# Kernel optimization log

Hardware: AMD Instinct MI355X
Metric: run time of the kernel (lower is better)

Reference implementation:

```python
import math
import jax, jax.numpy as jnp
import numpy as np

L, NH, DF = 4, 4, 32  # num_layers, num_heads, head_dim (H=128)
EPS = 1e-5


def ln(x, g, b):
    m = x.mean(-1, keepdims=True)
    v = ((x - m) ** 2).mean(-1, keepdims=True)
    return (x - m) * jax.lax.rsqrt(v + EPS) * g + b


def mha(x, w_in, b_in, w_out, b_out):
    # torch nn.MultiheadAttention self-attention, batch_first, no mask
    B, S, H = x.shape
    q, k, v = jnp.split(x @ w_in + b_in, 3, axis=-1)
    q = q.reshape(B, S, NH, DF)
    k = k.reshape(B, S, NH, DF)
    v = v.reshape(B, S, NH, DF)
    s = jnp.einsum('bqhd,bkhd->bhqk', q, k) / math.sqrt(DF)
    a = jax.nn.softmax(s, axis=-1)
    o = jnp.einsum('bhqk,bkhd->bqhd', a, v).reshape(B, S, H)
    return o @ w_out + b_out


def _forward(X_k, time_embed, step_embed, W_tr, b_tr, W_in, b_in, g_in, be_in,
             W_e, b_e, aw, ab, ow, ob, tng, tnb, f1w, f1b, f2w, f2b, fng, fnb,
             Wq, Wk, Wv, Wo, bo, Wem, bem, Wea, bea, e1w, e1b, e2w, e2b,
             gng, gnb, eng, enb, W_out, b_out, k_index, edge_index):
    B, N, T1, Cin = X_k.shape
    H = W_in.shape[1]
    # --- precompute_graph: self-loops + structural edge features ---
    loop = jnp.arange(N, dtype=edge_index.dtype)
    ei = jnp.concatenate([edge_index, jnp.stack([loop, loop])], axis=1)
    dst, src = ei[0], ei[1]
    E = ei.shape[1]
    deg = jnp.zeros((N,), jnp.float32).at[dst].add(1.0)
    deg_max = jnp.maximum(deg.max(), 1.0)
    edge_w = 1.0 / jnp.maximum(deg[dst], 1.0)
    feat = jnp.stack([edge_w, deg[src] / deg_max, deg[dst] / deg_max], axis=1)  # [E,3]
    # --- input embedding ---
    t_emb = time_embed  # [T1, te] (lookup of arange(T1) = whole table)
    X = jnp.concatenate(
        [X_k, jnp.broadcast_to(t_emb[None, None], (B, N, T1, t_emb.shape[-1]))], axis=-1)
    h = ln(X @ W_in + b_in, g_in, be_in)
    h = h + step_embed[k_index][:, None, None, :]
    e = feat @ W_e + b_e                       # [E, de]
    t_re = t_emb @ W_tr + b_tr                 # [T1, H]
    BT = B * T1
    for l in range(L):
        # temporal attention over T1
        h_flat = h.reshape(B * N, T1, H)
        attn_out = mha(h_flat, aw[l], ab[l], ow[l], ob[l])
        h = ln(h + attn_out.reshape(B, N, T1, H), tng[l], tnb[l])
        ffn = jax.nn.gelu(h @ f1w[l] + f1b[l], approximate=False) @ f2w[l] + f2b[l]
        h = ln(h + ffn, fng[l], fnb[l])
        h = h + t_re[None, None]
        # DiGress GT sparse graph block over N
        h_BT = h.transpose(0, 2, 1, 3).reshape(BT, N, H)
        Q = (h_BT @ Wq[l]).reshape(BT, N, NH, DF)
        K = (h_BT @ Wk[l]).reshape(BT, N, NH, DF)
        V = (h_BT @ Wv[l]).reshape(BT, N, NH, DF)
        scores = (Q[:, dst] * K[:, src]).sum(-1) / math.sqrt(DF)  # [BT,E,NH]
        scores = scores * (e @ Wem[l] + bem[l] + 1.0) + (e @ Wea[l] + bea[l])
        s_max = jax.lax.stop_gradient(scores.max(axis=1, keepdims=True))
        exp_s = jnp.exp(scores - s_max)
        denom = jnp.zeros((BT, N, NH), exp_s.dtype).at[:, dst, :].add(exp_s)
        attn = exp_s / (denom[:, dst, :] + 1e-9)
        agg = (attn[..., None] * V[:, src]).reshape(BT, E, H)
        out = jnp.zeros((BT, N, H), h.dtype).at[:, dst, :].add(agg)
        h_BT = h_BT + out @ Wo[l] + bo[l]
        h_mean = jax.lax.stop_gradient(h_BT).mean(0)               # [N,H]
        e_in = jnp.concatenate([h_mean[dst], h_mean[src], e], axis=-1)
        e_mlp = jax.nn.gelu(e_in @ e1w[l] + e1b[l], approximate=False) @ e2w[l] + e2b[l]
        e = ln(e + e_mlp, eng[l], enb[l])
        h = ln(h_BT.reshape(B, T1, N, H).transpose(0, 2, 1, 3), gng[l], gnb[l])
    return jax.nn.softmax(h @ W_out + b_out, axis=-1)


def setup_inputs() -> dict:
    key = jax.random.key(0)
    B, N, T1 = 2, 2000, 12
    sd, cc, te, H, de, nh = 4, 2, 16, 128, 16, 4
    Cin = (1 + cc) * sd  # 12
    E0, max_steps = 32000, 1024
    ks = iter(jax.random.split(key, 60))
    def rn(*shape, s=0.05):
        return jax.random.normal(next(ks), shape, jnp.float32) * s
    z = lambda *s: jnp.zeros(s, jnp.float32)
    o = lambda *s: jnp.ones(s, jnp.float32)
    return dict(
        X_k=jax.random.normal(next(ks), (B, N, T1, Cin), jnp.float32),
        time_embed=rn(T1, te), step_embed=rn(max_steps, H),
        W_tr=rn(te, H), b_tr=z(H),
        W_in=rn(Cin + te, H), b_in=z(H), g_in=o(H), be_in=z(H),
        W_e=rn(3, de), b_e=z(de),
        aw=rn(L, H, 3 * H), ab=z(L, 3 * H), ow=rn(L, H, H), ob=z(L, H),
        tng=o(L, H), tnb=z(L, H),
        f1w=rn(L, H, 2 * H), f1b=z(L, 2 * H), f2w=rn(L, 2 * H, H), f2b=z(L, H),
        fng=o(L, H), fnb=z(L, H),
        Wq=rn(L, H, H), Wk=rn(L, H, H), Wv=rn(L, H, H),
        Wo=rn(L, H, H), bo=z(L, H),
        Wem=rn(L, de, nh), bem=z(L, nh), Wea=rn(L, de, nh), bea=z(L, nh),
        e1w=rn(L, 2 * H + de, 4 * de), e1b=z(L, 4 * de),
        e2w=rn(L, 4 * de, de), e2b=z(L, de),
        gng=o(L, H), gnb=z(L, H), eng=o(L, de), enb=z(L, de),
        W_out=rn(H, sd), b_out=z(sd),
        k_index=jax.random.randint(next(ks), (B,), 0, max_steps),
        edge_index=jax.random.randint(next(ks), (2, E0), 0, N),
    )


def reference(X_k, time_embed, step_embed, W_tr, b_tr, W_in, b_in, g_in, be_in,
              W_e, b_e, aw, ab, ow, ob, tng, tnb, f1w, f1b, f2w, f2b, fng, fnb,
              Wq, Wk, Wv, Wo, bo, Wem, bem, Wea, bea, e1w, e1b, e2w, e2b,
              gng, gnb, eng, enb, W_out, b_out, k_index, edge_index):
    return _forward(X_k, time_embed, step_embed, W_tr, b_tr, W_in, b_in, g_in, be_in,
                    W_e, b_e, aw, ab, ow, ob, tng, tnb, f1w, f1b, f2w, f2b, fng, fnb,
                    Wq, Wk, Wv, Wo, bo, Wem, bem, Wea, bea, e1w, e1b, e2w, e2b,
                    gng, gnb, eng, enb, W_out, b_out, k_index, edge_index)
```

## Files before the change

### kernel.cpp

```cpp
#include <hip/hip_runtime.h>
#include <math.h>

#define NN 2000
#define T1C 12
#define BBC 2
#define HHC 128
#define NHD 4
#define DFD 32
#define LLC 4
#define DEC 16
#define TEC 16
#define CINC 12
#define E0C 32000
#define EEC 34000
#define BTC 24
#define MROWS 48000
#define EPSLN 1e-5f
#define SCALEQK 0.17677669529663687f

typedef __attribute__((ext_vector_type(8))) short short8;
typedef __attribute__((ext_vector_type(4))) float f32x4;


__device__ __forceinline__ unsigned short f2b(float f)
{
    unsigned u = __float_as_uint(f);
    return (unsigned short)((u + 0x7FFF + ((u >> 16) & 1)) >> 16);
}

__device__ __forceinline__ float b2f(unsigned short h)
{
    return __uint_as_float(((unsigned)h) << 16);
}


__global__ __launch_bounds__(256) void convwp_k(const float* __restrict__ W, unsigned short* __restrict__ Bp,
                                                int LN_, int K, int N, int noff, int Ntot)
{
    int idx = blockIdx.x * blockDim.x + threadIdx.x;
    int total = LN_ * K * N;
    if (idx >= total) return;
    int l = idx / (K * N);
    int r = idx - l * (K * N);
    int k = r / N;
    int n = r - k * N + noff;
    size_t off = (size_t)l * K * Ntot +
                 ((size_t)((n >> 4) * (K >> 5) + (k >> 5)) << 9) +
                 (((k >> 3) & 3) << 7) + ((n & 15) << 3) + (k & 7);
    Bp[off] = f2b(W[idx]);
}

__global__ __launch_bounds__(256) void convw12_k(const float* __restrict__ e1w, unsigned short* __restrict__ W12P)
{
    int idx = blockIdx.x * blockDim.x + threadIdx.x;
    if (idx >= LLC * 128 * 128) return;
    int l = idx >> 14;
    int r = idx & 16383;
    int c = r >> 7, k = r & 127;
    int sk = (c < 64) ? k : k + 128;
    int sc = c & 63;
    W12P[idx] = f2b(e1w[((size_t)l * 272 + sk) * 64 + sc]);
}

__global__ __launch_bounds__(256) void convwoT_k(const float* __restrict__ Wo, unsigned short* __restrict__ WoT)
{
    int idx = blockIdx.x * blockDim.x + threadIdx.x;
    if (idx >= LLC * 128 * 128) return;
    int l = idx >> 14;
    int r = idx & 16383;
    int c = r >> 7, k = r & 127;
    WoT[idx] = f2b(Wo[((size_t)l * 128 + k) * 128 + c]);
}


template<int K, int EPI, int OUTM>
__global__ __launch_bounds__(256) void gemm2_k(
    const unsigned short* __restrict__ A, const unsigned short* __restrict__ Bp,
    const float* __restrict__ bias, float* __restrict__ C, unsigned short* __restrict__ Cb,
    const float* __restrict__ res, const float* __restrict__ gam, const float* __restrict__ bet,
    const float* __restrict__ trep,
    int M, int Ntot)
{
    __shared__ unsigned short A_s[128 * 16 * 8];
    __shared__ float red2[2][128][2];

    int tid = threadIdx.x;
    int w = tid >> 6, lane = tid & 63;
    int wr = w & 1, wc = w >> 1;
    int quad = lane >> 4, lr = lane & 15;

    const unsigned short* abase = A + (size_t)blockIdx.x * 128 * K;
    int ntg0 = blockIdx.y * 8 + wc * 4;

    f32x4 acc[4][4];
#pragma unroll
    for (int mt = 0; mt < 4; mt++)
#pragma unroll
        for (int nt = 0; nt < 4; nt++) acc[mt][nt] = (f32x4){0.f, 0.f, 0.f, 0.f};

#pragma unroll
    for (int kb = 0; kb < K; kb += 128) {
        if (kb) __syncthreads();
#pragma unroll
        for (int j = 0; j < 8; j++) {
            int s = j * 256 + tid;
            int row = s >> 4, ks = s & 15;
            int ko = ks ^ (row & 15);
            uint4 d = *(const uint4*)(abase + (size_t)row * K + kb + ko * 8);
            *(uint4*)(A_s + s * 8) = d;
        }
        __syncthreads();
#pragma unroll
        for (int k0 = 0; k0 < 128; k0 += 32) {
            short8 af[4], bf[4];
#pragma unroll
            for (int mt = 0; mt < 4; mt++) {
                int row_l = wr * 64 + mt * 16 + lr;
                int koct = (k0 >> 3) + quad;
                int slot = row_l * 16 + (koct ^ lr);
                af[mt] = *(const short8*)(A_s + slot * 8);
            }
#pragma unroll
            for (int nt = 0; nt < 4; nt++) {
                size_t off = ((size_t)(ntg0 + nt) * (K >> 5) + ((kb + k0) >> 5)) * 512 + lane * 8;
                bf[nt] = *(const short8*)(Bp + off);
            }
#pragma unroll
            for (int mt = 0; mt < 4; mt++)
#pragma unroll
                for (int nt = 0; nt < 4; nt++)
                    acc[mt][nt] = __builtin_amdgcn_mfma_f32_16x16x32_bf16(af[mt], bf[nt], acc[mt][nt], 0, 0, 0);
        }
    }

    int rbase = blockIdx.x * 128 + wr * 64;
    int cbase = blockIdx.y * 128 + wc * 64;

    if constexpr (EPI != 3 && EPI != 4 && EPI != 5) {
#pragma unroll
        for (int mt = 0; mt < 4; mt++) {
#pragma unroll
            for (int nt = 0; nt < 4; nt++) {
                int colg = cbase + nt * 16 + lr;
                float bv = bias ? bias[colg] : 0.f;
#pragma unroll
                for (int i = 0; i < 4; i++) {
                    int row = rbase + mt * 16 + quad * 4 + i;
                    float x = acc[mt][nt][i] + bv;
                    if constexpr (EPI == 1) x = 0.5f * x * (1.f + erff(x * 0.70710678118654752f));
                    if constexpr (EPI == 2) x = res[(size_t)row * Ntot + colg] + x;
                    if constexpr (OUTM & 1) C[(size_t)row * Ntot + colg] = x;
                    if constexpr (OUTM & 4)
                        Cb[(size_t)blockIdx.y * M * 128 + (size_t)row * 128 + (wc * 64 + nt * 16 + lr)] = f2b(x);
                    else if constexpr (OUTM & 2)
                        Cb[(size_t)row * Ntot + colg] = f2b(x);
                }
            }
        }
    } else {
        float s[4][4], s2l[4][4];
#pragma unroll
        for (int mt = 0; mt < 4; mt++)
#pragma unroll
            for (int i = 0; i < 4; i++) { s[mt][i] = 0.f; s2l[mt][i] = 0.f; }
#pragma unroll
        for (int mt = 0; mt < 4; mt++) {
#pragma unroll
            for (int nt = 0; nt < 4; nt++) {
                int colg = cbase + nt * 16 + lr;
                float bv = bias[colg];
#pragma unroll
                for (int i = 0; i < 4; i++) {
                    int row = rbase + mt * 16 + quad * 4 + i;
                    float x = acc[mt][nt][i] + bv + res[(size_t)row * 128 + colg];
                    acc[mt][nt][i] = x;
                    s[mt][i] += x;
                    s2l[mt][i] += x * x;
                }
            }
        }
#pragma unroll
        for (int m = 1; m < 16; m <<= 1) {
#pragma unroll
            for (int mt = 0; mt < 4; mt++)
#pragma unroll
                for (int i = 0; i < 4; i++) {
                    s[mt][i]  += __shfl_xor(s[mt][i], m, 64);
                    s2l[mt][i] += __shfl_xor(s2l[mt][i], m, 64);
                }
        }
        if (lr == 0) {
#pragma unroll
            for (int mt = 0; mt < 4; mt++)
#pragma unroll
                for (int i = 0; i < 4; i++) {
                    int rl = wr * 64 + mt * 16 + quad * 4 + i;
                    red2[wc][rl][0] = s[mt][i];
                    red2[wc][rl][1] = s2l[mt][i];
                }
        }
        __syncthreads();
#pragma unroll
        for (int mt = 0; mt < 4; mt++) {
#pragma unroll
            for (int i = 0; i < 4; i++) {
                int rl = wr * 64 + mt * 16 + quad * 4 + i;
                float st  = red2[0][rl][0] + red2[1][rl][0];
                float s2t = red2[0][rl][1] + red2[1][rl][1];
                float mu = st * (1.f / 128.f);
                float rstd = rsqrtf(s2t * (1.f / 128.f) - mu * mu + EPSLN);
                int row = rbase + mt * 16 + quad * 4 + i;
                if constexpr (EPI == 4) {
                    int t = row % T1C;
                    int bn = row / T1C;
                    int b = bn / NN;
                    int n = bn - b * NN;
                    size_t rowp = (size_t)(b * T1C + t) * NN + n;
                    const float* trow = trep + t * HHC;
#pragma unroll
                    for (int nt = 0; nt < 4; nt++) {
                        int colg = cbase + nt * 16 + lr;
                        float y = (acc[mt][nt][i] - mu) * rstd * gam[colg] + bet[colg] + trow[colg];
                        C[rowp * 128 + colg] = y;
                        Cb[rowp * 128 + colg] = f2b(y);
                    }
                } else if constexpr (EPI == 5) {
                    int bt = row / NN, n = row - bt * NN;
                    int b = bt / T1C, t = bt - b * T1C;
                    size_t rowp = ((size_t)(b * NN + n)) * T1C + t;
#pragma unroll
                    for (int nt = 0; nt < 4; nt++) {
                        int colg = cbase + nt * 16 + lr;
                        float y = (acc[mt][nt][i] - mu) * rstd * gam[colg] + bet[colg];
                        C[rowp * 128 + colg] = y;
                        Cb[rowp * 128 + colg] = f2b(y);
                    }
                } else {
#pragma unroll
                    for (int nt = 0; nt < 4; nt++) {
                        int colg = cbase + nt * 16 + lr;
                        float y = (acc[mt][nt][i] - mu) * rstd * gam[colg] + bet[colg];
                        if constexpr (OUTM & 1) C[(size_t)row * 128 + colg] = y;
                        if constexpr (OUTM & 2) Cb[(size_t)row * 128 + colg] = f2b(y);
                    }
                }
            }
        }
    }
}

template<int K, int EPI, int OUTM>
static void run_gemm2(const unsigned short* A, const unsigned short* Bp, const float* bias,
                      float* C, unsigned short* Cb, const float* res, const float* g, const float* be,
                      const float* trep, int M, int Ntot, hipStream_t stream)
{
    dim3 grid(M / 128, Ntot / 128);
    gemm2_k<K, EPI, OUTM><<<grid, 256, 0, stream>>>(A, Bp, bias, C, Cb, res, g, be, trep, M, Ntot);
}


template<int NT>
__global__ __launch_bounds__(256) void gemm_mfma_k(
    const unsigned short* __restrict__ A, const unsigned short* __restrict__ WT,
    float* __restrict__ C, int M, int K)
{
    const int Nc = NT * 32;
    int tid = threadIdx.x;
    int w = tid >> 6, lane = tid & 63;
    int wr = w & 1, wc = w >> 1;
    int r0 = blockIdx.x * 32 + wr * 16;
    int c0 = wc * NT * 16;
    int lr = lane & 15;
    int kq = (lane >> 4) * 8;
    int arow = r0 + lr; if (arow >= M) arow = M - 1;
    const unsigned short* ap = A + (size_t)arow * K + kq;
    const unsigned short* wp = WT + (size_t)(c0 + lr) * K + kq;

    f32x4 acc[NT];
#pragma unroll
    for (int t = 0; t < NT; t++) acc[t] = (f32x4){0.f, 0.f, 0.f, 0.f};

    for (int k0 = 0; k0 < K; k0 += 32) {
        short8 a = *(const short8*)(ap + k0);
#pragma unroll
        for (int t = 0; t < NT; t++) {
            short8 b = *(const short8*)(wp + (size_t)t * 16 * K + k0);
            acc[t] = __builtin_amdgcn_mfma_f32_16x16x32_bf16(a, b, acc[t], 0, 0, 0);
        }
    }

    int orow0 = r0 + (lane >> 4) * 4;
#pragma unroll
    for (int t = 0; t < NT; t++) {
        int col = c0 + t * 16 + lr;
#pragma unroll
        for (int i = 0; i < 4; i++) {
            int row = orow0 + i;
            if (row < M) C[(size_t)row * Nc + col] = acc[t][i];
        }
    }
}

__global__ __launch_bounds__(256) void gemm_hm_k(
    const unsigned short* __restrict__ A, const unsigned short* __restrict__ WT,
    const float* __restrict__ mA, const float* __restrict__ bo,
    unsigned short* __restrict__ hmb, int M, int K)
{
    const int NT = 4;
    int tid = threadIdx.x;
    int w = tid >> 6, lane = tid & 63;
    int wr = w & 1, wc = w >> 1;
    int r0 = blockIdx.x * 32 + wr * 16;
    int c0 = wc * NT * 16;
    int lr = lane & 15;
    int kq = (lane >> 4) * 8;
    int arow = r0 + lr; if (arow >= M) arow = M - 1;
    const unsigned short* ap = A + (size_t)arow * K + kq;
    const unsigned short* wp = WT + (size_t)(c0 + lr) * K + kq;

    f32x4 acc[NT];
#pragma unroll
    for (int t = 0; t < NT; t++) acc[t] = (f32x4){0.f, 0.f, 0.f, 0.f};

    for (int k0 = 0; k0 < K; k0 += 32) {
        short8 a = *(const short8*)(ap + k0);
#pragma unroll
        for (int t = 0; t < NT; t++) {
            short8 b = *(const short8*)(wp + (size_t)t * 16 * K + k0);
            acc[t] = __builtin_amdgcn_mfma_f32_16x16x32_bf16(a, b, acc[t], 0, 0, 0);
        }
    }

    int orow0 = r0 + (lane >> 4) * 4;
#pragma unroll
    for (int t = 0; t < NT; t++) {
        int col = c0 + t * 16 + lr;
#pragma unroll
        for (int i = 0; i < 4; i++) {
            int row = orow0 + i;
            if (row < M) {
                float x = acc[t][i] + mA[(size_t)row * 128 + col] + bo[col];
                hmb[(size_t)row * 128 + col] = f2b(x);
            }
        }
    }
}


__global__ __launch_bounds__(256) void emlp_k(const float* __restrict__ P12,
                                              const int* __restrict__ dst, const int* __restrict__ src,
                                              const float* __restrict__ e1wE, const float* __restrict__ e1b_l,
                                              const float* __restrict__ e2w_l, const float* __restrict__ e2b_l,
                                              const float* __restrict__ g, const float* __restrict__ be,
                                              float* __restrict__ e)
{
    __shared__ float tl[4][64];
    int wv = threadIdx.x >> 6, l = threadIdx.x & 63;
    int r = blockIdx.x * 4 + wv;
    int d = dst[r], s = src[r];
    const float* ep = e + (size_t)r * DEC;
    float t = P12[(size_t)d * 128 + l] + P12[(size_t)s * 128 + 64 + l] + e1b_l[l];
#pragma unroll
    for (int k = 0; k < DEC; k++) t += ep[k] * e1wE[k * 64 + l];
    t = 0.5f * t * (1.f + erff(t * 0.70710678118654752f));
    tl[wv][l] = t;
    __syncthreads();
    int c = l & 15, kq = l >> 4;
    float p = 0.f;
#pragma unroll
    for (int j = 0; j < 16; j++) p += tl[wv][kq * 16 + j] * e2w_l[(kq * 16 + j) * 16 + c];
    p += __shfl_xor(p, 16, 64);
    p += __shfl_xor(p, 32, 64);
    float x = p + e2b_l[c] + ep[c];
    float s1 = x, s2 = x * x;
#pragma unroll
    for (int m = 1; m < 16; m <<= 1) {
        s1 += __shfl_xor(s1, m, 64);
        s2 += __shfl_xor(s2, m, 64);
    }
    float mu = s1 * (1.f / 16.f);
    float rstd = rsqrtf(s2 * (1.f / 16.f) - mu * mu + EPSLN);
    float y = (x - mu) * rstd * g[c] + be[c];
    if (l < 16) e[(size_t)r * DEC + c] = y;
}


__global__ __launch_bounds__(256) void zero_deg_k(int* __restrict__ degi)
{
    int i = blockIdx.x * blockDim.x + threadIdx.x;
    if (i < NN) degi[i] = 0;
}

__global__ __launch_bounds__(256) void build_edges_k(const int* __restrict__ eidx,
                                                     int* __restrict__ dst, int* __restrict__ src,
                                                     int* __restrict__ degi)
{
    int e = blockIdx.x * blockDim.x + threadIdx.x;
    if (e >= EEC) return;
    int d, s;
    if (e < E0C) { d = eidx[e]; s = eidx[E0C + e]; }
    else { d = e - E0C; s = e - E0C; }
    dst[e] = d;
    src[e] = s;
    atomicAdd(&degi[d], 1);
}

__global__ __launch_bounds__(256) void scan_k(const int* __restrict__ degi, int* __restrict__ rowptr,
                                              int* __restrict__ cursor, float* __restrict__ degmaxf)
{
    __shared__ int ssum[256];
    __shared__ int smx[256];
    int tid = threadIdx.x;
    int vals[8];
    int s = 0, mx = 0;
    int base = tid * 8;
#pragma unroll
    for (int j = 0; j < 8; j++) {
        int idx = base + j;
        int v = (idx < NN) ? degi[idx] : 0;
        vals[j] = v; s += v; mx = max(mx, v);
    }
    ssum[tid] = s; smx[tid] = mx;
    __syncthreads();
    for (int off = 1; off < 256; off <<= 1) {
        int t = (tid >= off) ? ssum[tid - off] : 0;
        __syncthreads();
        ssum[tid] += t;
        __syncthreads();
    }
    for (int off = 128; off > 0; off >>= 1) {
        if (tid < off) smx[tid] = max(smx[tid], smx[tid + off]);
        __syncthreads();
    }
    if (tid == 0) *degmaxf = fmaxf((float)smx[0], 1.f);
    int running = ssum[tid] - s;
#pragma unroll
    for (int j = 0; j < 8; j++) {
        int idx = base + j;
        if (idx < NN) { rowptr[idx] = running; cursor[idx] = running; running += vals[j]; }
    }
    if (tid == 255) rowptr[NN] = ssum[255];
}

__global__ __launch_bounds__(256) void feat_k(const int* __restrict__ dst, const int* __restrict__ src,
                                              const int* __restrict__ degi, const float* __restrict__ degmaxf,
                                              int* __restrict__ cursor, int* __restrict__ srcCSR,
                                              int* __restrict__ epos,
                                              const float* __restrict__ We, const float* __restrict__ bE,
                                              float* __restrict__ e)
{
    int ei = blockIdx.x * blockDim.x + threadIdx.x;
    if (ei >= EEC) return;
    int d = dst[ei], s = src[ei];
    int pos = atomicAdd(&cursor[d], 1);
    srcCSR[pos] = s;
    epos[ei] = pos;
    float dm = *degmaxf;
    float degd = (float)degi[d], degs = (float)degi[s];
    float f0 = 1.f / fmaxf(degd, 1.f);
    float f1 = degs / dm, f2 = degd / dm;
#pragma unroll
    for (int c = 0; c < DEC; c++)
        e[ei * DEC + c] = bE[c] + f0 * We[c] + f1 * We[DEC + c] + f2 * We[2 * DEC + c];
}


__global__ __launch_bounds__(256) void embed_k(const float* __restrict__ Xk, const float* __restrict__ temb,
                                               const float* __restrict__ Win, const float* __restrict__ bin,
                                               const float* __restrict__ g, const float* __restrict__ be,
                                               const float* __restrict__ stepemb, const int* __restrict__ kidx,
                                               float* __restrict__ h, unsigned short* __restrict__ hb)
{
    int row = blockIdx.x * 4 + (threadIdx.x >> 6);
    int l = threadIdx.x & 63;
    int t = row % T1C;
    int bn = row / T1C;
    int b = bn / NN;
    const float* xk = Xk + (size_t)row * CINC;
    const float* tp = temb + t * TEC;
    float acc0 = bin[l], acc1 = bin[l + 64];
#pragma unroll
    for (int k = 0; k < CINC; k++) {
        float xv = xk[k];
        acc0 += xv * Win[k * HHC + l];
        acc1 += xv * Win[k * HHC + l + 64];
    }
#pragma unroll
    for (int k = 0; k < TEC; k++) {
        float xv = tp[k];
        acc0 += xv * Win[(CINC + k) * HHC + l];
        acc1 += xv * Win[(CINC + k) * HHC + l + 64];
    }
    float s = acc0 + acc1, s2 = acc0 * acc0 + acc1 * acc1;
#pragma unroll
    for (int m = 32; m >= 1; m >>= 1) {
        s  += __shfl_xor(s, m, 64);
        s2 += __shfl_xor(s2, m, 64);
    }
    float mu = s * (1.f / 128.f);
    float rstd = rsqrtf(s2 * (1.f / 128.f) - mu * mu + EPSLN);
    const float* se = stepemb + (size_t)kidx[b] * HHC;
    float v0 = (acc0 - mu) * rstd * g[l] + be[l] + se[l];
    float v1 = (acc1 - mu) * rstd * g[l + 64] + be[l + 64] + se[l + 64];
    size_t ob = (size_t)row * HHC;
    h[ob + l] = v0;
    h[ob + l + 64] = v1;
    hb[ob + l] = f2b(v0);
    hb[ob + l + 64] = f2b(v1);
}

__global__ __launch_bounds__(128) void tre_k(const float* __restrict__ temb, const float* __restrict__ Wtr,
                                             const float* __restrict__ btr, float* __restrict__ tre)
{
    int t = blockIdx.x, c = threadIdx.x;
    float acc = btr[c];
#pragma unroll
    for (int k = 0; k < TEC; k++) acc += temb[t * TEC + k] * Wtr[k * HHC + c];
    tre[t * HHC + c] = acc;
}


__global__ __launch_bounds__(128) void temporal_attn_k(const unsigned short* __restrict__ qkvb,
                                                       unsigned short* __restrict__ outb)
{
    int bn = blockIdx.x;
    __shared__ unsigned short qkv_s[T1C][408];
    __shared__ float s[NHD][T1C][T1C];
    int tid = threadIdx.x;
    int hh = tid >> 5, lane = tid & 31;
    const unsigned short* base = qkvb + (size_t)bn * T1C * 384;
    for (int cIdx = tid; cIdx < 576; cIdx += 128) {
        uint4 d = *(const uint4*)(base + cIdx * 8);
        int t = cIdx / 48;
        int c0 = (cIdx - t * 48) * 8;
        *(uint4*)(&qkv_s[t][c0]) = d;
    }
    __syncthreads();
    for (int idx = lane; idx < T1C * T1C; idx += 32) {
        int tq = idx / T1C, tk = idx - tq * T1C;
        const unsigned* qp = (const unsigned*)&qkv_s[tq][hh * 32];
        const unsigned* kp = (const unsigned*)&qkv_s[tk][128 + hh * 32];
        float acc = 0.f;
#pragma unroll
        for (int d = 0; d < 16; d++) {
            unsigned a = qp[d], b = kp[d];
            acc += __uint_as_float(a << 16) * __uint_as_float(b << 16);
            acc += __uint_as_float(a & 0xFFFF0000u) * __uint_as_float(b & 0xFFFF0000u);
        }
        s[hh][tq][tk] = acc * SCALEQK;
    }
    __syncthreads();
    if (tid < NHD * T1C) {
        int h2 = tid / T1C, tq = tid - h2 * T1C;
        float mx = -1e30f;
#pragma unroll
        for (int j = 0; j < T1C; j++) mx = fmaxf(mx, s[h2][tq][j]);
        float sum = 0.f;
#pragma unroll
        for (int j = 0; j < T1C; j++) { float ex = __expf(s[h2][tq][j] - mx); s[h2][tq][j] = ex; sum += ex; }
        float inv = 1.f / sum;
#pragma unroll
        for (int j = 0; j < T1C; j++) s[h2][tq][j] *= inv;
    }
    __syncthreads();
    int oc = hh * 32 + lane;
#pragma unroll
    for (int t = 0; t < T1C; t++) {
        float acc = 0.f;
#pragma unroll
        for (int tk = 0; tk < T1C; tk++) acc += s[hh][t][tk] * b2f(qkv_s[tk][256 + oc]);
        outb[((size_t)bn * T1C + t) * HHC + oc] = f2b(acc);
    }
}


__global__ __launch_bounds__(256) void emea_k(const float* __restrict__ e, const int* __restrict__ epos,
                                              const float* __restrict__ Wem, const float* __restrict__ bem,
                                              const float* __restrict__ Wea, const float* __restrict__ bea,
                                              float* __restrict__ ec)
{
    int r = blockIdx.x * blockDim.x + threadIdx.x;
    if (r >= EEC) return;
    float ev[DEC];
#pragma unroll
    for (int k = 0; k < DEC; k++) ev[k] = e[r * DEC + k];
    int pos = epos[r];
#pragma unroll
    for (int hh = 0; hh < NHD; hh++) {
        float a = bem[hh], b2 = bea[hh];
#pragma unroll
        for (int k = 0; k < DEC; k++) { a += ev[k] * Wem[k * NHD + hh]; b2 += ev[k] * Wea[k * NHD + hh]; }
        ec[(size_t)pos * 8 + hh * 2]     = (a + 1.f) * SCALEQK;
        ec[(size_t)pos * 8 + hh * 2 + 1] = b2;
    }
}

__global__ __launch_bounds__(256) void sagg_k(const unsigned short* __restrict__ Q,
                                              const unsigned short* __restrict__ K,
                                              const unsigned short* __restrict__ V,
                                              const int* __restrict__ rowptr, const int* __restrict__ srcCSR,
                                              const float* __restrict__ ec, unsigned short* __restrict__ outb)
{
    int wv = threadIdx.x >> 6;
    int lane = threadIdx.x & 63;
    int blk = blockIdx.x;
    int bt = blk % BTC;
    int n  = (blk / BTC) * 4 + wv;
    int cg = lane & 15;
    int es = lane >> 4;
    int hh = cg >> 2;
    size_t base = (size_t)bt * NN;
    uint4 qd = *(const uint4*)(Q + (base + n) * HHC + cg * 8);
    unsigned qv[4] = {qd.x, qd.y, qd.z, qd.w};
    float q[8];
#pragma unroll
    for (int jj = 0; jj < 4; jj++) {
        q[2 * jj]     = __uint_as_float(qv[jj] << 16);
        q[2 * jj + 1] = __uint_as_float(qv[jj] & 0xFFFF0000u);
    }
    int s0 = rowptr[n], s1 = rowptr[n + 1];
    float acc[8];
#pragma unroll
    for (int j = 0; j < 8; j++) acc[j] = 0.f;
    float den = 0.f;
    for (int i = s0 + es; i < s1; i += 4) {
        int sn = srcCSR[i];
        uint4 kd = *(const uint4*)(K + (base + sn) * HHC + cg * 8);
        uint4 vd = *(const uint4*)(V + (base + sn) * HHC + cg * 8);
        float2 c2 = *(const float2*)(ec + (size_t)i * 8 + hh * 2);
        unsigned kv[4] = {kd.x, kd.y, kd.z, kd.w};
        float p = 0.f;
#pragma unroll
        for (int jj = 0; jj < 4; jj++) {
            p += q[2 * jj]     * __uint_as_float(kv[jj] << 16);
            p += q[2 * jj + 1] * __uint_as_float(kv[jj] & 0xFFFF0000u);
        }
        p += __shfl_xor(p, 1, 64);
        p += __shfl_xor(p, 2, 64);
        float w = __expf(p * c2.x + c2.y);
        unsigned vv[4] = {vd.x, vd.y, vd.z, vd.w};
#pragma unroll
        for (int jj = 0; jj < 4; jj++) {
            acc[2 * jj]     += w * __uint_as_float(vv[jj] << 16);
            acc[2 * jj + 1] += w * __uint_as_float(vv[jj] & 0xFFFF0000u);
        }
        den += w;
    }
#pragma unroll
    for (int j = 0; j < 8; j++) {
        acc[j] += __shfl_xor(acc[j], 16, 64);
        acc[j] += __shfl_xor(acc[j], 32, 64);
    }
    den += __shfl_xor(den, 16, 64);
    den += __shfl_xor(den, 32, 64);
    if (es == 0) {
        float inv = den + 1e-9f;
        unsigned short r[8];
#pragma unroll
        for (int j = 0; j < 8; j++) r[j] = f2b(acc[j] / inv);
        *(uint4*)(outb + (base + n) * HHC + cg * 8) = *(uint4*)r;
    }
}

__global__ __launch_bounds__(128) void hmean2_k(const float* __restrict__ hBT,
                                                const unsigned short* __restrict__ aggb,
                                                float* __restrict__ mA, unsigned short* __restrict__ mBb)
{
    int n = blockIdx.x, c = threadIdx.x;
    float sA = 0.f, sB = 0.f;
#pragma unroll
    for (int bt = 0; bt < BTC; bt++) {
        size_t off = ((size_t)bt * NN + n) * HHC + c;
        sA += hBT[off];
        sB += b2f(aggb[off]);
    }
    mA[n * HHC + c] = sA * (1.f / BTC);
    mBb[n * HHC + c] = f2b(sB * (1.f / BTC));
}


__global__ __launch_bounds__(256) void out_k(const float* __restrict__ h, const float* __restrict__ Wout,
                                             const float* __restrict__ bout, float* __restrict__ out)
{
    int row = blockIdx.x * 4 + (threadIdx.x >> 6);
    int lane = threadIdx.x & 63;
    const float* hp = h + (size_t)row * HHC;
    float x0 = hp[lane], x1 = hp[lane + 64];
    float w00 = Wout[lane * 4 + 0], w01 = Wout[lane * 4 + 1];
    float w02 = Wout[lane * 4 + 2], w03 = Wout[lane * 4 + 3];
    float w10 = Wout[(lane + 64) * 4 + 0], w11 = Wout[(lane + 64) * 4 + 1];
    float w12 = Wout[(lane + 64) * 4 + 2], w13 = Wout[(lane + 64) * 4 + 3];
    float p0 = x0 * w00 + x1 * w10;
    float p1 = x0 * w01 + x1 * w11;
    float p2 = x0 * w02 + x1 * w12;
    float p3 = x0 * w03 + x1 * w13;
#pragma unroll
    for (int m = 32; m >= 1; m >>= 1) {
        p0 += __shfl_xor(p0, m, 64);
        p1 += __shfl_xor(p1, m, 64);
        p2 += __shfl_xor(p2, m, 64);
        p3 += __shfl_xor(p3, m, 64);
    }
    if (lane == 0) {
        float l0 = p0 + bout[0], l1 = p1 + bout[1], l2 = p2 + bout[2], l3 = p3 + bout[3];
        float mx = fmaxf(fmaxf(l0, l1), fmaxf(l2, l3));
        float e0 = __expf(l0 - mx), e1 = __expf(l1 - mx), e2 = __expf(l2 - mx), e3 = __expf(l3 - mx);
        float inv = 1.f / (e0 + e1 + e2 + e3);
        float4 o = {e0 * inv, e1 * inv, e2 * inv, e3 * inv};
        *(float4*)(out + (size_t)row * 4) = o;
    }
}


extern "C" void kernel_launch(void* const* d_in, const int* in_sizes, int n_in,
                              void* d_out, int out_size, void* d_ws, size_t ws_size,
                              hipStream_t stream)
{
    const float* Xk      = (const float*)d_in[0];
    const float* temb    = (const float*)d_in[1];
    const float* stepemb = (const float*)d_in[2];
    const float* Wtr     = (const float*)d_in[3];
    const float* btr     = (const float*)d_in[4];
    const float* Win     = (const float*)d_in[5];
    const float* bin     = (const float*)d_in[6];
    const float* gin     = (const float*)d_in[7];
    const float* bein    = (const float*)d_in[8];
    const float* We      = (const float*)d_in[9];
    const float* bE      = (const float*)d_in[10];
    const float* aw      = (const float*)d_in[11];
    const float* ab      = (const float*)d_in[12];
    const float* ow      = (const float*)d_in[13];
    const float* ob      = (const float*)d_in[14];
    const float* tng     = (const float*)d_in[15];
    const float* tnb     = (const float*)d_in[16];
    const float* f1w     = (const float*)d_in[17];
    const float* f1b     = (const float*)d_in[18];
    const float* f2w     = (const float*)d_in[19];
    const float* f2b_    = (const float*)d_in[20];
    const float* fng     = (const float*)d_in[21];
    const float* fnb     = (const float*)d_in[22];
    const float* Wq      = (const float*)d_in[23];
    const float* Wk      = (const float*)d_in[24];
    const float* Wv      = (const float*)d_in[25];
    const float* Wo      = (const float*)d_in[26];
    const float* bo      = (const float*)d_in[27];
    const float* Wem     = (const float*)d_in[28];
    const float* bem     = (const float*)d_in[29];
    const float* Wea     = (const float*)d_in[30];
    const float* bea     = (const float*)d_in[31];
    const float* e1w     = (const float*)d_in[32];
    const float* e1b     = (const float*)d_in[33];
    const float* e2w     = (const float*)d_in[34];
    const float* e2b     = (const float*)d_in[35];
    const float* gng     = (const float*)d_in[36];
    const float* gnb     = (const float*)d_in[37];
    const float* eng     = (const float*)d_in[38];
    const float* enb     = (const float*)d_in[39];
    const float* Wout    = (const float*)d_in[40];
    const float* bout    = (const float*)d_in[41];
    const int*   kidx    = (const int*)d_in[42];
    const int*   eidx    = (const int*)d_in[43];
    float* outp = (float*)d_out;

    char* wsp = (char*)d_ws;
    auto alloc = [&](size_t nbytes) -> void* {
        void* p = (void*)wsp;
        wsp += (nbytes + 255) & ~(size_t)255;
        return p;
    };
    float* h     = (float*)alloc((size_t)MROWS * HHC * 4);
    unsigned short* hb = (unsigned short*)alloc((size_t)MROWS * HHC * 2);
    float* hBT   = (float*)alloc((size_t)MROWS * HHC * 4);
    unsigned short* hBTb = (unsigned short*)alloc((size_t)MROWS * HHC * 2);
    float* bufC  = (float*)alloc((size_t)MROWS * 384 * 4);
    unsigned short* bufDb = (unsigned short*)alloc((size_t)MROWS * HHC * 2);
    float* ebuf  = (float*)alloc((size_t)EEC * DEC * 4);
    float* ec    = (float*)alloc((size_t)EEC * NHD * 2 * 4);
    float* P12   = (float*)alloc((size_t)NN * HHC * 4);
    float* mA    = (float*)alloc((size_t)NN * HHC * 4);
    unsigned short* mBb = (unsigned short*)alloc((size_t)NN * HHC * 2);
    unsigned short* hmb = (unsigned short*)alloc((size_t)NN * HHC * 2);
    float* tre   = (float*)alloc((size_t)T1C * HHC * 4);
    float* degmaxf = (float*)alloc(4);
    int* degi   = (int*)alloc((size_t)NN * 4);
    int* dst    = (int*)alloc((size_t)EEC * 4);
    int* srcA   = (int*)alloc((size_t)EEC * 4);
    int* srcCSR = (int*)alloc((size_t)EEC * 4);
    int* epos   = (int*)alloc((size_t)EEC * 4);
    int* rowptr = (int*)alloc((size_t)(NN + 1) * 4);
    int* cursor = (int*)alloc((size_t)NN * 4);
    unsigned short* awP   = (unsigned short*)alloc((size_t)LLC * 384 * 128 * 2);
    unsigned short* owP   = (unsigned short*)alloc((size_t)LLC * 128 * 128 * 2);
    unsigned short* f1P   = (unsigned short*)alloc((size_t)LLC * 256 * 128 * 2);
    unsigned short* f2P   = (unsigned short*)alloc((size_t)LLC * 128 * 256 * 2);
    unsigned short* WqkvP = (unsigned short*)alloc((size_t)LLC * 384 * 128 * 2);
    unsigned short* WoP   = (unsigned short*)alloc((size_t)LLC * 128 * 128 * 2);
    unsigned short* WoT   = (unsigned short*)alloc((size_t)LLC * 128 * 128 * 2);
    unsigned short* W12P  = (unsigned short*)alloc((size_t)LLC * 128 * 128 * 2);

    unsigned short* bufCb = (unsigned short*)bufC;
    unsigned short* midb  = (unsigned short*)bufC;
    unsigned short* Qc    = (unsigned short*)bufC;
    unsigned short* Kc    = Qc + (size_t)MROWS * HHC;
    unsigned short* Vc    = Kc + (size_t)MROWS * HHC;

    {
        auto cwp = [&](const float* W, unsigned short* Bp, int K, int N, int noff, int Ntot) {
            int total = LLC * K * N;
            convwp_k<<<(total + 255) / 256, 256, 0, stream>>>(W, Bp, LLC, K, N, noff, Ntot);
        };
        cwp(aw,  awP, 128, 384, 0, 384);
        cwp(ow,  owP, 128, 128, 0, 128);
        cwp(f1w, f1P, 128, 256, 0, 256);
        cwp(f2w, f2P, 256, 128, 0, 128);
        cwp(Wq,  WqkvP, 128, 128, 0,   384);
        cwp(Wk,  WqkvP, 128, 128, 128, 384);
        cwp(Wv,  WqkvP, 128, 128, 256, 384);
        cwp(Wo,  WoP, 128, 128, 0, 128);
        convwoT_k<<<(LLC * 128 * 128 + 255) / 256, 256, 0, stream>>>(Wo, WoT);
        convw12_k<<<(LLC * 128 * 128 + 255) / 256, 256, 0, stream>>>(e1w, W12P);
    }

    zero_deg_k<<<(NN + 255) / 256, 256, 0, stream>>>(degi);
    build_edges_k<<<(EEC + 255) / 256, 256, 0, stream>>>(eidx, dst, srcA, degi);
    scan_k<<<1, 256, 0, stream>>>(degi, rowptr, cursor, degmaxf);
    feat_k<<<(EEC + 255) / 256, 256, 0, stream>>>(dst, srcA, degi, degmaxf, cursor, srcCSR, epos, We, bE, ebuf);

    embed_k<<<MROWS / 4, 256, 0, stream>>>(Xk, temb, Win, bin, gin, bein, stepemb, kidx, h, hb);
    tre_k<<<T1C, 128, 0, stream>>>(temb, Wtr, btr, tre);

    for (int l = 0; l < LLC; l++) {
        const unsigned short* awP_l   = awP   + (size_t)l * 384 * 128;
        const unsigned short* owP_l   = owP   + (size_t)l * 128 * 128;
        const unsigned short* f1P_l   = f1P   + (size_t)l * 256 * 128;
        const unsigned short* f2P_l   = f2P   + (size_t)l * 128 * 256;
        const unsigned short* WqkvP_l = WqkvP + (size_t)l * 384 * 128;
        const unsigned short* WoP_l   = WoP   + (size_t)l * 128 * 128;
        const unsigned short* WoT_l   = WoT   + (size_t)l * 128 * 128;
        const unsigned short* W12P_l  = W12P  + (size_t)l * 128 * 128;
        const float* ab_l  = ab  + (size_t)l * 3 * HHC;
        const float* ob_l  = ob  + (size_t)l * HHC;
        const float* tng_l = tng + (size_t)l * HHC;
        const float* tnb_l = tnb + (size_t)l * HHC;
        const float* f1b_l = f1b + (size_t)l * 256;
        const float* f2b_l = f2b_ + (size_t)l * HHC;
        const float* fng_l = fng + (size_t)l * HHC;
        const float* fnb_l = fnb + (size_t)l * HHC;
        const float* bo_l  = bo  + (size_t)l * HHC;
        const float* Wem_l = Wem + (size_t)l * DEC * NHD;
        const float* bem_l = bem + (size_t)l * NHD;
        const float* Wea_l = Wea + (size_t)l * DEC * NHD;
        const float* bea_l = bea + (size_t)l * NHD;
        const float* e1wE_l = e1w + ((size_t)l * 272 + 256) * 64;
        const float* e1b_l = e1b + (size_t)l * 64;
        const float* e2w_l = e2w + (size_t)l * 64 * DEC;
        const float* e2b_l = e2b + (size_t)l * DEC;
        const float* gng_l = gng + (size_t)l * HHC;
        const float* gnb_l = gnb + (size_t)l * HHC;
        const float* eng_l = eng + (size_t)l * DEC;
        const float* enb_l = enb + (size_t)l * DEC;

        run_gemm2<128, 0, 2>(hb, awP_l, ab_l, nullptr, bufCb, nullptr, nullptr, nullptr, nullptr, MROWS, 384, stream);
        temporal_attn_k<<<BBC * NN, 128, 0, stream>>>(bufCb, bufDb);
        run_gemm2<128, 3, 3>(bufDb, owP_l, ob_l, h, hb, h, tng_l, tnb_l, nullptr, MROWS, 128, stream);
        run_gemm2<128, 1, 2>(hb, f1P_l, f1b_l, nullptr, midb, nullptr, nullptr, nullptr, nullptr, MROWS, 256, stream);
        run_gemm2<256, 4, 3>(midb, f2P_l, f2b_l, hBT, hBTb, h, fng_l, fnb_l, tre, MROWS, 128, stream);
        run_gemm2<128, 0, 4>(hBTb, WqkvP_l, nullptr, nullptr, Qc, nullptr, nullptr, nullptr, nullptr, MROWS, 384, stream);
        emea_k<<<(EEC + 255) / 256, 256, 0, stream>>>(ebuf, epos, Wem_l, bem_l, Wea_l, bea_l, ec);
        sagg_k<<<BTC * (NN / 4), 256, 0, stream>>>(Qc, Kc, Vc, rowptr, srcCSR, ec, bufDb);
        hmean2_k<<<NN, 128, 0, stream>>>(hBT, bufDb, mA, mBb);
        run_gemm2<128, 5, 3>(bufDb, WoP_l, bo_l, h, hb, hBT, gng_l, gnb_l, nullptr, MROWS, 128, stream);
        gemm_hm_k<<<(NN + 31) / 32, 256, 0, stream>>>(mBb, WoT_l, mA, bo_l, hmb, NN, 128);
        gemm_mfma_k<4><<<(NN + 31) / 32, 256, 0, stream>>>(hmb, W12P_l, P12, NN, 128);
        emlp_k<<<EEC / 4, 256, 0, stream>>>(P12, dst, srcA, e1wE_l, e1b_l, e2w_l, e2b_l, eng_l, enb_l, ebuf);
    }

    out_k<<<MROWS / 4, 256, 0, stream>>>(h, Wout, bout, outp);
}
```

Measured before the change: 1.089 ms.

## Fuse FFN up-projection, GELU and down-projection into one kernel

Replaces the two separate FFN GEMM launches with a single kernel. It computes the 256-wide GELU intermediate in two 128-column halves kept in shared memory and accumulates the down-projection in registers, then applies the residual, LayerNorm and time-embedding epilogue with the transposed row store. This removes the global-memory round trip of the 48000x256 bf16 intermediate and one launch. In exchange each block does more serial work with a larger register footprint, and the grid is only 375 blocks, which may reduce occupancy and latency hiding.

```diff
diff --git a/kernel.cpp b/kernel.cpp
--- a/kernel.cpp
+++ b/kernel.cpp
@@ -256,6 +256,185 @@
 {
     dim3 grid(M / 128, Ntot / 128);
     gemm2_k<K, EPI, OUTM><<<grid, 256, 0, stream>>>(A, Bp, bias, C, Cb, res, g, be, trep, M, Ntot);
+}
+
+
+__global__ __launch_bounds__(256) void ffn_k(
+    const unsigned short* __restrict__ A,
+    const unsigned short* __restrict__ F1p,
+    const unsigned short* __restrict__ F2p,
+    const float* __restrict__ f1b_l, const float* __restrict__ f2b_l,
+    const float* __restrict__ res,
+    const float* __restrict__ gam, const float* __restrict__ bet,
+    const float* __restrict__ trep,
+    float* __restrict__ C, unsigned short* __restrict__ Cb)
+{
+    __shared__ unsigned short A_s[128 * 16 * 8];
+    __shared__ unsigned short M_s[128 * 16 * 8];
+    __shared__ float red2[2][128][2];
+
+    int tid = threadIdx.x;
+    int w = tid >> 6, lane = tid & 63;
+    int wr = w & 1, wc = w >> 1;
+    int quad = lane >> 4, lr = lane & 15;
+
+    const unsigned short* abase = A + (size_t)blockIdx.x * 128 * 128;
+
+#pragma unroll
+    for (int j = 0; j < 8; j++) {
+        int s = j * 256 + tid;
+        int row = s >> 4, ks = s & 15;
+        int ko = ks ^ (row & 15);
+        uint4 d = *(const uint4*)(abase + (size_t)row * 128 + ko * 8);
+        *(uint4*)(A_s + s * 8) = d;
+    }
+    __syncthreads();
+
+    f32x4 facc[4][4];
+#pragma unroll
+    for (int mt = 0; mt < 4; mt++)
+#pragma unroll
+        for (int nt = 0; nt < 4; nt++) facc[mt][nt] = (f32x4){0.f, 0.f, 0.f, 0.f};
+
+#pragma unroll
+    for (int half = 0; half < 2; half++) {
+        f32x4 macc[4][4];
+#pragma unroll
+        for (int mt = 0; mt < 4; mt++)
+#pragma unroll
+            for (int nt = 0; nt < 4; nt++) macc[mt][nt] = (f32x4){0.f, 0.f, 0.f, 0.f};
+#pragma unroll
+        for (int k0 = 0; k0 < 128; k0 += 32) {
+            short8 af[4], bf[4];
+#pragma unroll
+            for (int mt = 0; mt < 4; mt++) {
+                int row_l = wr * 64 + mt * 16 + lr;
+                int koct = (k0 >> 3) + quad;
+                int slot = row_l * 16 + (koct ^ lr);
+                af[mt] = *(const short8*)(A_s + slot * 8);
+            }
+#pragma unroll
+            for (int nt = 0; nt < 4; nt++) {
+                size_t off = ((size_t)(half * 8 + wc * 4 + nt) * 4 + (k0 >> 5)) * 512 + lane * 8;
+                bf[nt] = *(const short8*)(F1p + off);
+            }
+#pragma unroll
+            for (int mt = 0; mt < 4; mt++)
+#pragma unroll
+                for (int nt = 0; nt < 4; nt++)
+                    macc[mt][nt] = __builtin_amdgcn_mfma_f32_16x16x32_bf16(af[mt], bf[nt], macc[mt][nt], 0, 0, 0);
+        }
+        if (half) __syncthreads();
+#pragma unroll
+        for (int mt = 0; mt < 4; mt++) {
+#pragma unroll
+            for (int nt = 0; nt < 4; nt++) {
+                int col = wc * 64 + nt * 16 + lr;
+                float bv = f1b_l[half * 128 + col];
+                int cchunk = col >> 3, celem = col & 7;
+#pragma unroll
+                for (int i = 0; i < 4; i++) {
+                    int row = wr * 64 + mt * 16 + quad * 4 + i;
+                    float x = macc[mt][nt][i] + bv;
+                    x = 0.5f * x * (1.f + erff(x * 0.70710678118654752f));
+                    int ks = cchunk ^ (row & 15);
+                    M_s[(row * 16 + ks) * 8 + celem] = f2b(x);
+                }
+            }
+        }
+        __syncthreads();
+#pragma unroll
+        for (int k0 = 0; k0 < 128; k0 += 32) {
+            short8 af[4], bf[4];
+#pragma unroll
+            for (int mt = 0; mt < 4; mt++) {
+                int row_l = wr * 64 + mt * 16 + lr;
+                int koct = (k0 >> 3) + quad;
+                int slot = row_l * 16 + (koct ^ lr);
+                af[mt] = *(const short8*)(M_s + slot * 8);
+            }
+#pragma unroll
+            for (int nt = 0; nt < 4; nt++) {
+                size_t off = ((size_t)(wc * 4 + nt) * 8 + ((half * 128 + k0) >> 5)) * 512 + lane * 8;
+                bf[nt] = *(const short8*)(F2p + off);
+            }
+#pragma unroll
+            for (int mt = 0; mt < 4; mt++)
+#pragma unroll
+                for (int nt = 0; nt < 4; nt++)
+                    facc[mt][nt] = __builtin_amdgcn_mfma_f32_16x16x32_bf16(af[mt], bf[nt], facc[mt][nt], 0, 0, 0);
+        }
+    }
+
+    int rbase = blockIdx.x * 128 + wr * 64;
+    int cbase = wc * 64;
+    float s[4][4], s2l[4][4];
+#pragma unroll
+    for (int mt = 0; mt < 4; mt++)
+#pragma unroll
+        for (int i = 0; i < 4; i++) { s[mt][i] = 0.f; s2l[mt][i] = 0.f; }
+#pragma unroll
+    for (int mt = 0; mt < 4; mt++) {
+#pragma unroll
+        for (int nt = 0; nt < 4; nt++) {
+            int colg = cbase + nt * 16 + lr;
+            float bv = f2b_l[colg];
+#pragma unroll
+            for (int i = 0; i < 4; i++) {
+                int row = rbase + mt * 16 + quad * 4 + i;
+                float x = facc[mt][nt][i] + bv + res[(size_t)row * 128 + colg];
+                facc[mt][nt][i] = x;
+                s[mt][i] += x;
+                s2l[mt][i] += x * x;
+            }
+        }
+    }
+#pragma unroll
+    for (int m = 1; m < 16; m <<= 1) {
+#pragma unroll
+        for (int mt = 0; mt < 4; mt++)
+#pragma unroll
+            for (int i = 0; i < 4; i++) {
+                s[mt][i]  += __shfl_xor(s[mt][i], m, 64);
+                s2l[mt][i] += __shfl_xor(s2l[mt][i], m, 64);
+            }
+    }
+    if (lr == 0) {
+#pragma unroll
+        for (int mt = 0; mt < 4; mt++)
+#pragma unroll
+            for (int i = 0; i < 4; i++) {
+                int rl = wr * 64 + mt * 16 + quad * 4 + i;
+                red2[wc][rl][0] = s[mt][i];
+                red2[wc][rl][1] = s2l[mt][i];
+            }
+    }
+    __syncthreads();
+#pragma unroll
+    for (int mt = 0; mt < 4; mt++) {
+#pragma unroll
+        for (int i = 0; i < 4; i++) {
+            int rl = wr * 64 + mt * 16 + quad * 4 + i;
+            float st  = red2[0][rl][0] + red2[1][rl][0];
+            float s2t = red2[0][rl][1] + red2[1][rl][1];
+            float mu = st * (1.f / 128.f);
+            float rstd = rsqrtf(s2t * (1.f / 128.f) - mu * mu + EPSLN);
+            int row = rbase + mt * 16 + quad * 4 + i;
+            int t = row % T1C;
+            int bn = row / T1C;
+            int b = bn / NN;
+            int n = bn - b * NN;
+            size_t rowp = (size_t)(b * T1C + t) * NN + n;
+            const float* trow = trep + t * HHC;
+#pragma unroll
+            for (int nt = 0; nt < 4; nt++) {
+                int colg = cbase + nt * 16 + lr;
+                float y = (facc[mt][nt][i] - mu) * rstd * gam[colg] + bet[colg] + trow[colg];
+                C[rowp * 128 + colg] = y;
+                Cb[rowp * 128 + colg] = f2b(y);
+            }
+        }
+    }
 }
 
 
@@ -799,7 +978,6 @@
     unsigned short* W12P  = (unsigned short*)alloc((size_t)LLC * 128 * 128 * 2);
 
     unsigned short* bufCb = (unsigned short*)bufC;
-    unsigned short* midb  = (unsigned short*)bufC;
     unsigned short* Qc    = (unsigned short*)bufC;
     unsigned short* Kc    = Qc + (size_t)MROWS * HHC;
     unsigned short* Vc    = Kc + (size_t)MROWS * HHC;
@@ -863,8 +1041,8 @@
         run_gemm2<128, 0, 2>(hb, awP_l, ab_l, nullptr, bufCb, nullptr, nullptr, nullptr, nullptr, MROWS, 384, stream);
         temporal_attn_k<<<BBC * NN, 128, 0, stream>>>(bufCb, bufDb);
         run_gemm2<128, 3, 3>(bufDb, owP_l, ob_l, h, hb, h, tng_l, tnb_l, nullptr, MROWS, 128, stream);
-        run_gemm2<128, 1, 2>(hb, f1P_l, f1b_l, nullptr, midb, nullptr, nullptr, nullptr, nullptr, MROWS, 256, stream);
-        run_gemm2<256, 4, 3>(midb, f2P_l, f2b_l, hBT, hBTb, h, fng_l, fnb_l, tre, MROWS, 128, stream);
+        ffn_k<<<MROWS / 128, 256, 0, stream>>>(hb, f1P_l, f2P_l, f1b_l, f2b_l, h,
+                                               fng_l, fnb_l, tre, hBT, hBTb);
         run_gemm2<128, 0, 4>(hBTb, WqkvP_l, nullptr, nullptr, Qc, nullptr, nullptr, nullptr, nullptr, MROWS, 384, stream);
         emea_k<<<(EEC + 255) / 256, 256, 0, stream>>>(ebuf, epos, Wem_l, bem_l, Wea_l, bea_l, ec);
         sagg_k<<<BTC * (NN / 4), 256, 0, stream>>>(Qc, Kc, Vc, rowptr, srcCSR, ec, bufDb);
```

New measurement: 1.154 ms. 6.0% more time.
